# Performance work log

Hardware: AMD Instinct MI355X
Metric: run time of the kernel (lower is better)

Reference implementation:

```python
import jax, jax.numpy as jnp
import numpy as np

N_NODES = 50000
N_EDGES = 800000
IN_DIM, HIDDEN, Z_DIM = 32, 64, 32


def gcn_conv(x, W, b, src, dst, n):
    """PyG-style GCNConv: h = D^{-1/2}(A+I)D^{-1/2} (x W) + b."""
    h = x @ W  # [N, out]
    loop = jnp.arange(n, dtype=src.dtype)
    s = jnp.concatenate([src, loop])  # add self-loops
    d = jnp.concatenate([dst, loop])
    deg = jax.ops.segment_sum(jnp.ones(s.shape, h.dtype), d, num_segments=n)
    dinv = jax.lax.rsqrt(jnp.maximum(deg, jnp.asarray(1.0, h.dtype)))
    norm = dinv[s] * dinv[d]                       # [E+N]
    msg = h[s] * norm[:, None]                     # gather + scale
    out = jax.ops.segment_sum(msg, d, num_segments=n)  # scatter-add
    return out + b


def setup_inputs() -> dict:
    key = jax.random.key(0)
    ks = jax.random.split(key, 8)
    sc = lambda fan_in: 1.0 / np.sqrt(fan_in)
    x = jax.random.normal(ks[0], (N_NODES, IN_DIM), jnp.float32)
    edge_index = jax.random.randint(ks[1], (2, N_EDGES), 0, N_NODES, jnp.int64)
    W1 = jax.random.normal(ks[2], (IN_DIM, HIDDEN), jnp.float32) * sc(IN_DIM)
    b1 = jnp.zeros((HIDDEN,), jnp.float32)
    W2 = jax.random.normal(ks[3], (HIDDEN, HIDDEN), jnp.float32) * sc(HIDDEN)
    b2 = jnp.zeros((HIDDEN,), jnp.float32)
    W_mu = jax.random.normal(ks[4], (HIDDEN, Z_DIM), jnp.float32) * sc(HIDDEN)
    b_mu = jnp.zeros((Z_DIM,), jnp.float32)
    W_lv = jax.random.normal(ks[5], (HIDDEN, Z_DIM), jnp.float32) * sc(HIDDEN)
    b_lv = jnp.zeros((Z_DIM,), jnp.float32)
    eps = jax.random.normal(ks[6], (N_NODES, Z_DIM), jnp.float32)
    return {"x": x, "edge_index": edge_index, "W1": W1, "b1": b1, "W2": W2,
            "b2": b2, "W_mu": W_mu, "b_mu": b_mu, "W_lv": W_lv, "b_lv": b_lv,
            "eps": eps}


def reference(x, edge_index, W1, b1, W2, b2, W_mu, b_mu, W_lv, b_lv, eps):
    src, dst = edge_index[0], edge_index[1]
    n = x.shape[0]
    h = jax.nn.relu(gcn_conv(x, W1, b1, src, dst, n))
    h = jax.nn.relu(gcn_conv(h, W2, b2, src, dst, n))
    # dropout p=0.0 -> identity
    mu = gcn_conv(h, W_mu, b_mu, src, dst, n)
    logvar = gcn_conv(h, W_lv, b_lv, src, dst, n)
    z = mu + jnp.exp(0.5 * logvar) * eps  # reparametrize
    return (z, mu, logvar)
```

## Files before the change

### kernel.cpp

```cpp
#include <hip/hip_runtime.h>
#include <math.h>

#define N_NODES 50000
#define N_EDGES 800000
#define IN_DIM 32
#define HIDDEN 64
#define Z_DIM 32
#define SCAN_B 256
#define NB_SCAN ((N_NODES + SCAN_B - 1) / SCAN_B)
#define N_XCD 8
#define NPX ((N_NODES + N_XCD - 1) / N_XCD)
#define SLICE 2048
#define N_SLICE ((N_EDGES + SLICE - 1) / SLICE)
#define SCAT_B (N_SLICE * N_XCD)
#define FB 2048

__device__ __forceinline__ float bf2f(unsigned short u) {
    return __uint_as_float(((unsigned int)u) << 16);
}
__device__ __forceinline__ unsigned short f2bf(float f) {
    unsigned int u = __float_as_uint(f);
    u += 0x7fffu + ((u >> 16) & 1u);
    return (unsigned short)(u >> 16);
}

__device__ __forceinline__ int detect64(const int* raw) {
    int lane = threadIdx.x & 63;
    int odd = raw[2 * lane + 1];
    unsigned long long b = __ballot(odd != 0);
    return (b == 0ULL) ? 1 : 0;
}

__global__ void prep_kernel(const float* __restrict__ x, unsigned short* __restrict__ xb,
                            const void* __restrict__ raw, int* __restrict__ flag,
                            int* __restrict__ cnt, int2* __restrict__ ep0) {
    int is64 = detect64((const int*)raw);
    int i = blockIdx.x * 256 + threadIdx.x;
    if (blockIdx.x == 0 && threadIdx.x == 0) *flag = is64;
    if (i < N_NODES * IN_DIM) xb[i] = f2bf(x[i]);
    if (blockIdx.x < SCAT_B) {
        int xcd = blockIdx.x % N_XCD;
        int sl  = blockIdx.x / N_XCD;
        int own = ((sl % N_XCD) == xcd) ? 1 : 0;
        int lo  = xcd * NPX, hi = lo + NPX;
        int base = sl * SLICE;
#pragma unroll
        for (int j = 0; j < SLICE / 256; j++) {
            int e = base + j * 256 + threadIdx.x;
            if (e < N_EDGES) {
                int d = is64 ? (int)((const long long*)raw)[N_EDGES + e]
                             : ((const int*)raw)[N_EDGES + e];
                if (own) {
                    int s = is64 ? (int)((const long long*)raw)[e]
                                 : ((const int*)raw)[e];
                    ep0[e] = make_int2(s, d);
                }
                if (d >= lo && d < hi) atomicAdd(&cnt[d], 1);
            }
        }
    }
}

__global__ void scan1_kernel(const int* __restrict__ cnt, int* __restrict__ pre,
                             int* __restrict__ bsum, float* __restrict__ dinv) {
    __shared__ int s[SCAN_B];
    int t = threadIdx.x;
    int g = blockIdx.x * SCAN_B + t;
    int v = (g < N_NODES) ? cnt[g] : 0;
    if (g < N_NODES) dinv[g] = rsqrtf((float)(v + 1));
    s[t] = v;
    __syncthreads();
    for (int o = 1; o < SCAN_B; o <<= 1) {
        int add = (t >= o) ? s[t - o] : 0;
        __syncthreads();
        s[t] += add;
        __syncthreads();
    }
    if (g < N_NODES) pre[g] = s[t] - v;
    if (t == SCAN_B - 1) bsum[blockIdx.x] = s[t];
}

__global__ void scan23_kernel(int* __restrict__ rowptr, const int* __restrict__ bsum,
                              int* __restrict__ cursor) {
    __shared__ int s[256];
    int t = threadIdx.x;
    int v = (t < NB_SCAN) ? bsum[t] : 0;
    s[t] = v;
    __syncthreads();
    for (int o = 1; o < 256; o <<= 1) {
        int add = (t >= o) ? s[t - o] : 0;
        __syncthreads();
        s[t] += add;
        __syncthreads();
    }
    int excl = s[blockIdx.x] - bsum[blockIdx.x];
    int g = blockIdx.x * SCAN_B + t;
    if (g < N_NODES) {
        int r = rowptr[g] + excl;
        rowptr[g] = r;
        cursor[g] = r;
    }
    if (g == 0) rowptr[N_NODES] = N_EDGES;
}

__global__ __launch_bounds__(256) void scatter_kernel(
        const int2* __restrict__ ep0, const float* __restrict__ dinv,
        int* __restrict__ cursor, int2* __restrict__ ep) {
    int xcd = blockIdx.x % N_XCD;
    int sl  = blockIdx.x / N_XCD;
    int lo  = xcd * NPX, hi = lo + NPX;
    int base = sl * SLICE;
#pragma unroll
    for (int j = 0; j < SLICE / 256; j++) {
        int e = base + j * 256 + threadIdx.x;
        if (e >= N_EDGES) continue;
        int2 sd = ep0[e];
        if (sd.y >= lo && sd.y < hi) {
            float w = dinv[sd.x];
            int p = atomicAdd(&cursor[sd.y], 1);
            ep[p] = make_int2(sd.x, __float_as_int(w));
        }
    }
}

__device__ __forceinline__ float2 agg_node64(int e0, int e1, int2 pr0,
                                             const int2* __restrict__ ep,
                                             const unsigned int* __restrict__ gw,
                                             int lane, float2 acc) {
    int half = lane >> 5;
    int col  = lane & 31;
    int2 pr = pr0;
    for (int base = e0; base < e1; base += 64) {
        int cnt = e1 - base; cnt = cnt > 64 ? 64 : cnt;
        int j = 0;
        for (; j + 16 <= cnt; j += 16) {
            unsigned int fv[8]; float wv[8];
#pragma unroll
            for (int u = 0; u < 8; u++) {
                int j0 = j + 2 * u;
                int sa = __builtin_amdgcn_readlane(pr.x, j0);
                int sb = __builtin_amdgcn_readlane(pr.x, j0 + 1);
                int wa = __builtin_amdgcn_readlane(pr.y, j0);
                int wb = __builtin_amdgcn_readlane(pr.y, j0 + 1);
                int s  = half ? sb : sa;
                wv[u]  = __int_as_float(half ? wb : wa);
                fv[u]  = gw[(size_t)s * 32 + col];
            }
#pragma unroll
            for (int u = 0; u < 8; u++) {
                acc.x = fmaf(wv[u], __uint_as_float(fv[u] << 16),          acc.x);
                acc.y = fmaf(wv[u], __uint_as_float(fv[u] & 0xffff0000u),  acc.y);
            }
        }
        for (; j < cnt; j += 8) {
            unsigned int fv[4]; float wv[4];
#pragma unroll
            for (int u = 0; u < 4; u++) {
                int j0 = j + 2 * u, j1 = j0 + 1;
                int ia = j0 < 63 ? j0 : 63;
                int ib = j1 < 63 ? j1 : 63;
                int sa = __builtin_amdgcn_readlane(pr.x, ia);
                int sb = __builtin_amdgcn_readlane(pr.x, ib);
                float wa = (j0 < cnt) ? __int_as_float(__builtin_amdgcn_readlane(pr.y, ia)) : 0.0f;
                float wb = (j1 < cnt) ? __int_as_float(__builtin_amdgcn_readlane(pr.y, ib)) : 0.0f;
                int s  = half ? sb : sa;
                wv[u]  = half ? wb : wa;
                fv[u]  = gw[(size_t)s * 32 + col];
            }
#pragma unroll
            for (int u = 0; u < 4; u++) {
                acc.x = fmaf(wv[u], __uint_as_float(fv[u] << 16),          acc.x);
                acc.y = fmaf(wv[u], __uint_as_float(fv[u] & 0xffff0000u),  acc.y);
            }
        }
        int nb = base + 64;
        if (nb < e1) {
            int idx = nb + lane;
            pr = ep[idx < N_EDGES ? idx : (N_EDGES - 1)];
        }
    }
    return acc;
}

__device__ __forceinline__ float2 agg_node32(int e0, int e1, int2 pr0,
                                             const int2* __restrict__ ep,
                                             const unsigned int* __restrict__ xw,
                                             int lane, float2 acc) {
    int qc  = lane >> 4;
    int col = lane & 15;
    int2 pr = pr0;
    for (int base = e0; base < e1; base += 64) {
        int cnt = e1 - base; cnt = cnt > 64 ? 64 : cnt;
        int j = 0;
        for (; j + 16 <= cnt; j += 16) {
            unsigned int fv[4]; float wv[4];
#pragma unroll
            for (int u = 0; u < 4; u++) {
                int j0 = j + 4 * u;
                int s0 = __builtin_amdgcn_readlane(pr.x, j0);
                int s1 = __builtin_amdgcn_readlane(pr.x, j0 + 1);
                int s2 = __builtin_amdgcn_readlane(pr.x, j0 + 2);
                int s3 = __builtin_amdgcn_readlane(pr.x, j0 + 3);
                int w0 = __builtin_amdgcn_readlane(pr.y, j0);
                int w1 = __builtin_amdgcn_readlane(pr.y, j0 + 1);
                int w2 = __builtin_amdgcn_readlane(pr.y, j0 + 2);
                int w3 = __builtin_amdgcn_readlane(pr.y, j0 + 3);
                int s  = qc == 0 ? s0 : qc == 1 ? s1 : qc == 2 ? s2 : s3;
                int w  = qc == 0 ? w0 : qc == 1 ? w1 : qc == 2 ? w2 : w3;
                wv[u]  = __int_as_float(w);
                fv[u]  = xw[(size_t)s * 16 + col];
            }
#pragma unroll
            for (int u = 0; u < 4; u++) {
                acc.x = fmaf(wv[u], __uint_as_float(fv[u] << 16),          acc.x);
                acc.y = fmaf(wv[u], __uint_as_float(fv[u] & 0xffff0000u),  acc.y);
            }
        }
        for (; j < cnt; j += 8) {
            unsigned int fv[2]; float wv[2];
#pragma unroll
            for (int u = 0; u < 2; u++) {
                int j0 = j + 4 * u;
                int i0 = j0     < 63 ? j0     : 63;
                int i1 = j0 + 1 < 63 ? j0 + 1 : 63;
                int i2 = j0 + 2 < 63 ? j0 + 2 : 63;
                int i3 = j0 + 3 < 63 ? j0 + 3 : 63;
                int s0 = __builtin_amdgcn_readlane(pr.x, i0);
                int s1 = __builtin_amdgcn_readlane(pr.x, i1);
                int s2 = __builtin_amdgcn_readlane(pr.x, i2);
                int s3 = __builtin_amdgcn_readlane(pr.x, i3);
                float w0 = (j0     < cnt) ? __int_as_float(__builtin_amdgcn_readlane(pr.y, i0)) : 0.0f;
                float w1 = (j0 + 1 < cnt) ? __int_as_float(__builtin_amdgcn_readlane(pr.y, i1)) : 0.0f;
                float w2 = (j0 + 2 < cnt) ? __int_as_float(__builtin_amdgcn_readlane(pr.y, i2)) : 0.0f;
                float w3 = (j0 + 3 < cnt) ? __int_as_float(__builtin_amdgcn_readlane(pr.y, i3)) : 0.0f;
                int s  = qc == 0 ? s0 : qc == 1 ? s1 : qc == 2 ? s2 : s3;
                wv[u]  = qc == 0 ? w0 : qc == 1 ? w1 : qc == 2 ? w2 : w3;
                fv[u]  = xw[(size_t)s * 16 + col];
            }
#pragma unroll
            for (int u = 0; u < 2; u++) {
                acc.x = fmaf(wv[u], __uint_as_float(fv[u] << 16),          acc.x);
                acc.y = fmaf(wv[u], __uint_as_float(fv[u] & 0xffff0000u),  acc.y);
            }
        }
        int nb = base + 64;
        if (nb < e1) {
            int idx = nb + lane;
            pr = ep[idx < N_EDGES ? idx : (N_EDGES - 1)];
        }
    }
    return acc;
}

__global__ __launch_bounds__(256, 4) void fused_layer32_kernel(
        const int* __restrict__ rowptr, const int2* __restrict__ ep,
        const float* __restrict__ dinv, const unsigned short* __restrict__ xb,
        const float* __restrict__ W1, const float* __restrict__ b1,
        unsigned short* __restrict__ out) {
    __shared__ float sq[4 * 64];
    int lane = threadIdx.x & 63;
    int wav  = threadIdx.x >> 6;
    int qc   = lane >> 4;
    const unsigned int* xw = (const unsigned int*)xb;
    float wcol[IN_DIM];
#pragma unroll
    for (int k = 0; k < IN_DIM; k++) wcol[k] = W1[k * 64 + lane];
    float bb = b1[lane];
    int wid = __builtin_amdgcn_readfirstlane((int)((blockIdx.x * blockDim.x + threadIdx.x) >> 6));
    int nw  = (gridDim.x * blockDim.x) >> 6;
    int v = wid;
    if (v >= N_NODES) return;
    int e0 = rowptr[v], e1 = rowptr[v + 1];
    float dv = dinv[v];
    unsigned int hv = xw[(size_t)v * 16 + (lane & 15)];
    int i0 = e0 + lane;
    int2 pr = ep[i0 < N_EDGES ? i0 : (N_EDGES - 1)];
    while (v < N_NODES) {
        int vn = v + nw;
        int e0n = 0, e1n = 0;
        float dvn = 0.0f;
        unsigned int hvn = 0;
        int2 prn = make_int2(0, 0);
        if (vn < N_NODES) {
            e0n = rowptr[vn]; e1n = rowptr[vn + 1];
            dvn = dinv[vn];
            hvn = xw[(size_t)vn * 16 + (lane & 15)];
            int in0 = e0n + lane;
            prn = ep[in0 < N_EDGES ? in0 : (N_EDGES - 1)];
        }
        float sv = (qc == 0) ? dv : 0.0f;
        float2 acc;
        acc.x = sv * __uint_as_float(hv << 16);
        acc.y = sv * __uint_as_float(hv & 0xffff0000u);
        acc = agg_node32(e0, e1, pr, ep, xw, lane, acc);
        acc.x += __shfl_xor(acc.x, 16);
        acc.y += __shfl_xor(acc.y, 16);
        acc.x += __shfl_xor(acc.x, 32);
        acc.y += __shfl_xor(acc.y, 32);
        float qx = dv * acc.x, qy = dv * acc.y;
        if (lane < 16) ((float2*)sq)[wav * 32 + lane] = make_float2(qx, qy);
        float o = bb;
        const float4* q4 = (const float4*)(sq + wav * 64);
#pragma unroll
        for (int c = 0; c < IN_DIM / 4; c++) {
            float4 t = q4[c];
            o = fmaf(t.x, wcol[4 * c + 0], o);
            o = fmaf(t.y, wcol[4 * c + 1], o);
            o = fmaf(t.z, wcol[4 * c + 2], o);
            o = fmaf(t.w, wcol[4 * c + 3], o);
        }
        out[(size_t)v * 64 + lane] = f2bf(fmaxf(o, 0.0f));
        v = vn; e0 = e0n; e1 = e1n; dv = dvn; hv = hvn; pr = prn;
    }
}

__global__ __launch_bounds__(256, 4) void fused_layer64_kernel(
        const int* __restrict__ rowptr, const int2* __restrict__ ep,
        const float* __restrict__ dinv, const unsigned short* __restrict__ g,
        const float* __restrict__ W, const float* __restrict__ bias,
        unsigned short* __restrict__ out) {
    __shared__ float sq[4 * 64];
    int lane = threadIdx.x & 63;
    int wav  = threadIdx.x >> 6;
    int half = lane >> 5;
    const unsigned int* gw = (const unsigned int*)g;
    float wcol[HIDDEN];
#pragma unroll
    for (int k = 0; k < HIDDEN; k++) wcol[k] = W[k * 64 + lane];
    float bb = bias[lane];
    int wid = __builtin_amdgcn_readfirstlane((int)((blockIdx.x * blockDim.x + threadIdx.x) >> 6));
    int nw  = (gridDim.x * blockDim.x) >> 6;
    int v = wid;
    if (v >= N_NODES) return;
    int e0 = rowptr[v], e1 = rowptr[v + 1];
    float dv = dinv[v];
    unsigned int hv = gw[(size_t)v * 32 + (lane & 31)];
    int i0 = e0 + lane;
    int2 pr = ep[i0 < N_EDGES ? i0 : (N_EDGES - 1)];
    while (v < N_NODES) {
        int vn = v + nw;
        int e0n = 0, e1n = 0;
        float dvn = 0.0f;
        unsigned int hvn = 0;
        int2 prn = make_int2(0, 0);
        if (vn < N_NODES) {
            e0n = rowptr[vn]; e1n = rowptr[vn + 1];
            dvn = dinv[vn];
            hvn = gw[(size_t)vn * 32 + (lane & 31)];
            int in0 = e0n + lane;
            prn = ep[in0 < N_EDGES ? in0 : (N_EDGES - 1)];
        }
        float sv = half ? 0.0f : dv;
        float2 acc;
        acc.x = sv * __uint_as_float(hv << 16);
        acc.y = sv * __uint_as_float(hv & 0xffff0000u);
        acc = agg_node64(e0, e1, pr, ep, gw, lane, acc);
        acc.x += __shfl_xor(acc.x, 32);
        acc.y += __shfl_xor(acc.y, 32);
        float qx = dv * acc.x, qy = dv * acc.y;
        if (lane < 32) ((float2*)sq)[wav * 32 + lane] = make_float2(qx, qy);
        float o = bb;
        const float4* q4 = (const float4*)(sq + wav * 64);
#pragma unroll
        for (int c = 0; c < HIDDEN / 4; c++) {
            float4 t = q4[c];
            o = fmaf(t.x, wcol[4 * c + 0], o);
            o = fmaf(t.y, wcol[4 * c + 1], o);
            o = fmaf(t.z, wcol[4 * c + 2], o);
            o = fmaf(t.w, wcol[4 * c + 3], o);
        }
        out[(size_t)v * 64 + lane] = f2bf(fmaxf(o, 0.0f));
        v = vn; e0 = e0n; e1 = e1n; dv = dvn; hv = hvn; pr = prn;
    }
}

__global__ __launch_bounds__(256, 4) void fused_head_kernel(
        const int* __restrict__ rowptr, const int2* __restrict__ ep,
        const float* __restrict__ dinv, const unsigned short* __restrict__ g,
        const float* __restrict__ Wmu, const float* __restrict__ Wlv,
        const float* __restrict__ bmu, const float* __restrict__ blv,
        const float* __restrict__ eps, float* __restrict__ outz) {
    __shared__ float sq[4 * 64];
    int lane = threadIdx.x & 63;
    int wav  = threadIdx.x >> 6;
    int half = lane >> 5;
    int f = lane & 31;
    bool hi = lane >= 32;
    const unsigned int* gw = (const unsigned int*)g;
    float wcol[HIDDEN];
#pragma unroll
    for (int k = 0; k < HIDDEN; k++)
        wcol[k] = hi ? Wlv[k * 32 + f] : Wmu[k * 32 + f];
    float bb = hi ? blv[f] : bmu[f];
    float* z  = outz;
    float* mu = outz + (size_t)N_NODES * Z_DIM;
    float* lv = outz + 2 * (size_t)N_NODES * Z_DIM;
    int wid = __builtin_amdgcn_readfirstlane((int)((blockIdx.x * blockDim.x + threadIdx.x) >> 6));
    int nw  = (gridDim.x * blockDim.x) >> 6;
    int v = wid;
    if (v >= N_NODES) return;
    int e0 = rowptr[v], e1 = rowptr[v + 1];
    float dv = dinv[v];
    unsigned int hv = gw[(size_t)v * 32 + (lane & 31)];
    int i0 = e0 + lane;
    int2 pr = ep[i0 < N_EDGES ? i0 : (N_EDGES - 1)];
    while (v < N_NODES) {
        int vn = v + nw;
        int e0n = 0, e1n = 0;
        float dvn = 0.0f;
        unsigned int hvn = 0;
        int2 prn = make_int2(0, 0);
        if (vn < N_NODES) {
            e0n = rowptr[vn]; e1n = rowptr[vn + 1];
            dvn = dinv[vn];
            hvn = gw[(size_t)vn * 32 + (lane & 31)];
            int in0 = e0n + lane;
            prn = ep[in0 < N_EDGES ? in0 : (N_EDGES - 1)];
        }
        float sv = half ? 0.0f : dv;
        float2 acc;
        acc.x = sv * __uint_as_float(hv << 16);
        acc.y = sv * __uint_as_float(hv & 0xffff0000u);
        acc = agg_node64(e0, e1, pr, ep, gw, lane, acc);
        acc.x += __shfl_xor(acc.x, 32);
        acc.y += __shfl_xor(acc.y, 32);
        float qx = dv * acc.x, qy = dv * acc.y;
        if (lane < 32) ((float2*)sq)[wav * 32 + lane] = make_float2(qx, qy);
        float m = bb;
        const float4* q4 = (const float4*)(sq + wav * 64);
#pragma unroll
        for (int c = 0; c < HIDDEN / 4; c++) {
            float4 t = q4[c];
            m = fmaf(t.x, wcol[4 * c + 0], m);
            m = fmaf(t.y, wcol[4 * c + 1], m);
            m = fmaf(t.z, wcol[4 * c + 2], m);
            m = fmaf(t.w, wcol[4 * c + 3], m);
        }
        float ev = eps[(size_t)v * Z_DIM + f];
        float t  = expf(0.5f * m) * ev;
        float tlo = __shfl(t, lane | 32);
        size_t o = (size_t)v * Z_DIM + f;
        if (!hi) { mu[o] = m; z[o] = m + tlo; }
        else     { lv[o] = m; }
        v = vn; e0 = e0n; e1 = e1n; dv = dvn; hv = hvn; pr = prn;
    }
}

extern "C" void kernel_launch(void* const* d_in, const int* in_sizes, int n_in,
                              void* d_out, int out_size, void* d_ws, size_t ws_size,
                              hipStream_t stream) {
    const float* x   = (const float*)d_in[0];
    const void*  ei  = d_in[1];
    const float* W1  = (const float*)d_in[2];
    const float* b1  = (const float*)d_in[3];
    const float* W2  = (const float*)d_in[4];
    const float* b2  = (const float*)d_in[5];
    const float* Wmu = (const float*)d_in[6];
    const float* bmu = (const float*)d_in[7];
    const float* Wlv = (const float*)d_in[8];
    const float* blv = (const float*)d_in[9];
    const float* eps = (const float*)d_in[10];
    float* out = (float*)d_out;
    (void)in_sizes; (void)n_in; (void)out_size; (void)ws_size;

    char* ws = (char*)d_ws;
    size_t off = 0;
    auto alloc = [&](size_t bytes) -> void* {
        void* p = ws + off;
        off += (bytes + 255) & ~(size_t)255;
        return p;
    };
    int2*           ep     = (int2*)alloc(sizeof(int2) * N_EDGES);
    int2*           ep0    = (int2*)alloc(sizeof(int2) * N_EDGES);
    int*            rowptr = (int*)alloc(sizeof(int) * (N_NODES + 1));
    int*            cursor = (int*)alloc(sizeof(int) * N_NODES);
    int*            cnt    = (int*)alloc(sizeof(int) * N_NODES);
    float*          dinv   = (float*)alloc(sizeof(float) * N_NODES);
    int*            flag   = (int*)alloc(sizeof(int) * 64);
    int*            bsum   = (int*)alloc(sizeof(int) * 256);
    unsigned short* xb     = (unsigned short*)alloc(sizeof(short) * (size_t)N_NODES * IN_DIM);
    unsigned short* G      = (unsigned short*)alloc(sizeof(short) * (size_t)N_NODES * HIDDEN);
    unsigned short* H      = (unsigned short*)alloc(sizeof(short) * (size_t)N_NODES * HIDDEN);

    hipMemsetAsync(cnt, 0, sizeof(int) * N_NODES, stream);
    prep_kernel<<<(N_NODES * IN_DIM + 255) / 256, 256, 0, stream>>>(x, xb, ei, flag, cnt, ep0);
    scan1_kernel<<<NB_SCAN, SCAN_B, 0, stream>>>(cnt, rowptr, bsum, dinv);
    scan23_kernel<<<NB_SCAN, SCAN_B, 0, stream>>>(rowptr, bsum, cursor);
    scatter_kernel<<<SCAT_B, 256, 0, stream>>>(ep0, dinv, cursor, ep);
    fused_layer32_kernel<<<FB, 256, 0, stream>>>(rowptr, ep, dinv, xb, W1, b1, H);
    fused_layer64_kernel<<<FB, 256, 0, stream>>>(rowptr, ep, dinv, H, W2, b2, G);
    fused_head_kernel<<<FB, 256, 0, stream>>>(rowptr, ep, dinv, G, Wmu, Wlv, bmu, blv, eps, out);
}
```

Before: 274.2 us.

## Record atomic rank in count pass; widen gather lanes to 8-byte loads

The degree-count pass now stores each edge's atomic return value as its rank, so the CSR scatter becomes a plain rowptr+rank write with no second atomic pass and no per-XCD filtering. The aggregation loops now give each lane 4 bf16 features through 8-byte loads, with more edges in flight per wave. Edge indices are broadcast with ds_bpermute instead of chains of readlane, and the tail loop is merged into the main loop using clamped indices. This costs an extra rank array and more shuffle reductions per node, and the scatter now spans all destinations, so its writes may have worse locality.

```diff
diff --git a/kernel.cpp b/kernel.cpp
--- a/kernel.cpp
+++ b/kernel.cpp
@@ -33,7 +33,8 @@
 
 __global__ void prep_kernel(const float* __restrict__ x, unsigned short* __restrict__ xb,
                             const void* __restrict__ raw, int* __restrict__ flag,
-                            int* __restrict__ cnt, int2* __restrict__ ep0) {
+                            int* __restrict__ cnt, int2* __restrict__ ep0,
+                            int* __restrict__ rank) {
     int is64 = detect64((const int*)raw);
     int i = blockIdx.x * 256 + threadIdx.x;
     if (blockIdx.x == 0 && threadIdx.x == 0) *flag = is64;
@@ -55,7 +56,7 @@
                                  : ((const int*)raw)[e];
                     ep0[e] = make_int2(s, d);
                 }
-                if (d >= lo && d < hi) atomicAdd(&cnt[d], 1);
+                if (d >= lo && d < hi) rank[e] = atomicAdd(&cnt[d], 1);
             }
         }
     }
@@ -80,8 +81,7 @@
     if (t == SCAN_B - 1) bsum[blockIdx.x] = s[t];
 }
 
-__global__ void scan23_kernel(int* __restrict__ rowptr, const int* __restrict__ bsum,
-                              int* __restrict__ cursor) {
+__global__ void scan23_kernel(int* __restrict__ rowptr, const int* __restrict__ bsum) {
     __shared__ int s[256];
     int t = threadIdx.x;
     int v = (t < NB_SCAN) ? bsum[t] : 0;
@@ -95,82 +95,51 @@
     }
     int excl = s[blockIdx.x] - bsum[blockIdx.x];
     int g = blockIdx.x * SCAN_B + t;
-    if (g < N_NODES) {
-        int r = rowptr[g] + excl;
-        rowptr[g] = r;
-        cursor[g] = r;
-    }
+    if (g < N_NODES) rowptr[g] += excl;
     if (g == 0) rowptr[N_NODES] = N_EDGES;
 }
 
 __global__ __launch_bounds__(256) void scatter_kernel(
-        const int2* __restrict__ ep0, const float* __restrict__ dinv,
-        int* __restrict__ cursor, int2* __restrict__ ep) {
-    int xcd = blockIdx.x % N_XCD;
-    int sl  = blockIdx.x / N_XCD;
-    int lo  = xcd * NPX, hi = lo + NPX;
-    int base = sl * SLICE;
+        const int2* __restrict__ ep0, const int* __restrict__ rank,
+        const int* __restrict__ rowptr, const float* __restrict__ dinv,
+        int2* __restrict__ ep) {
+    int base = blockIdx.x * SLICE;
 #pragma unroll
     for (int j = 0; j < SLICE / 256; j++) {
         int e = base + j * 256 + threadIdx.x;
-        if (e >= N_EDGES) continue;
-        int2 sd = ep0[e];
-        if (sd.y >= lo && sd.y < hi) {
-            float w = dinv[sd.x];
-            int p = atomicAdd(&cursor[sd.y], 1);
-            ep[p] = make_int2(sd.x, __float_as_int(w));
-        }
-    }
-}
-
-__device__ __forceinline__ float2 agg_node64(int e0, int e1, int2 pr0,
-                                             const int2* __restrict__ ep,
-                                             const unsigned int* __restrict__ gw,
-                                             int lane, float2 acc) {
-    int half = lane >> 5;
-    int col  = lane & 31;
-    int2 pr = pr0;
+        if (e < N_EDGES) {
+            int2 sd = ep0[e];
+            int p = rowptr[sd.y] + rank[e];
+            ep[p] = make_int2(sd.x, __float_as_int(dinv[sd.x]));
+        }
+    }
+}
+
+__device__ __forceinline__ void agg_body64(int e0, int e1, int2 pr,
+                                           const int2* __restrict__ ep,
+                                           const uint2* __restrict__ g2,
+                                           int lane, float acc[4]) {
+    int gsel = lane >> 4;
+    int c    = lane & 15;
     for (int base = e0; base < e1; base += 64) {
         int cnt = e1 - base; cnt = cnt > 64 ? 64 : cnt;
-        int j = 0;
-        for (; j + 16 <= cnt; j += 16) {
-            unsigned int fv[8]; float wv[8];
-#pragma unroll
-            for (int u = 0; u < 8; u++) {
-                int j0 = j + 2 * u;
-                int sa = __builtin_amdgcn_readlane(pr.x, j0);
-                int sb = __builtin_amdgcn_readlane(pr.x, j0 + 1);
-                int wa = __builtin_amdgcn_readlane(pr.y, j0);
-                int wb = __builtin_amdgcn_readlane(pr.y, j0 + 1);
-                int s  = half ? sb : sa;
-                wv[u]  = __int_as_float(half ? wb : wa);
-                fv[u]  = gw[(size_t)s * 32 + col];
+        for (int j = 0; j < cnt; j += 16) {
+            uint2 fv[4]; float wv[4];
+#pragma unroll
+            for (int u = 0; u < 4; u++) {
+                int idx = j + u * 4 + gsel;
+                int cl  = idx < cnt ? idx : cnt - 1;
+                int s   = __builtin_amdgcn_ds_bpermute(cl << 2, pr.x);
+                int w   = __builtin_amdgcn_ds_bpermute(cl << 2, pr.y);
+                wv[u]   = idx < cnt ? __int_as_float(w) : 0.0f;
+                fv[u]   = g2[(size_t)s * 16 + c];
             }
 #pragma unroll
-            for (int u = 0; u < 8; u++) {
-                acc.x = fmaf(wv[u], __uint_as_float(fv[u] << 16),          acc.x);
-                acc.y = fmaf(wv[u], __uint_as_float(fv[u] & 0xffff0000u),  acc.y);
-            }
-        }
-        for (; j < cnt; j += 8) {
-            unsigned int fv[4]; float wv[4];
-#pragma unroll
             for (int u = 0; u < 4; u++) {
-                int j0 = j + 2 * u, j1 = j0 + 1;
-                int ia = j0 < 63 ? j0 : 63;
-                int ib = j1 < 63 ? j1 : 63;
-                int sa = __builtin_amdgcn_readlane(pr.x, ia);
-                int sb = __builtin_amdgcn_readlane(pr.x, ib);
-                float wa = (j0 < cnt) ? __int_as_float(__builtin_amdgcn_readlane(pr.y, ia)) : 0.0f;
-                float wb = (j1 < cnt) ? __int_as_float(__builtin_amdgcn_readlane(pr.y, ib)) : 0.0f;
-                int s  = half ? sb : sa;
-                wv[u]  = half ? wb : wa;
-                fv[u]  = gw[(size_t)s * 32 + col];
-            }
-#pragma unroll
-            for (int u = 0; u < 4; u++) {
-                acc.x = fmaf(wv[u], __uint_as_float(fv[u] << 16),          acc.x);
-                acc.y = fmaf(wv[u], __uint_as_float(fv[u] & 0xffff0000u),  acc.y);
+                acc[0] = fmaf(wv[u], __uint_as_float(fv[u].x << 16),         acc[0]);
+                acc[1] = fmaf(wv[u], __uint_as_float(fv[u].x & 0xffff0000u), acc[1]);
+                acc[2] = fmaf(wv[u], __uint_as_float(fv[u].y << 16),         acc[2]);
+                acc[3] = fmaf(wv[u], __uint_as_float(fv[u].y & 0xffff0000u), acc[3]);
             }
         }
         int nb = base + 64;
@@ -179,68 +148,33 @@
             pr = ep[idx < N_EDGES ? idx : (N_EDGES - 1)];
         }
     }
-    return acc;
-}
-
-__device__ __forceinline__ float2 agg_node32(int e0, int e1, int2 pr0,
-                                             const int2* __restrict__ ep,
-                                             const unsigned int* __restrict__ xw,
-                                             int lane, float2 acc) {
-    int qc  = lane >> 4;
-    int col = lane & 15;
-    int2 pr = pr0;
+}
+
+__device__ __forceinline__ void agg_body32(int e0, int e1, int2 pr,
+                                           const int2* __restrict__ ep,
+                                           const uint2* __restrict__ x2,
+                                           int lane, float acc[4]) {
+    int gsel = lane >> 3;
+    int c    = lane & 7;
     for (int base = e0; base < e1; base += 64) {
         int cnt = e1 - base; cnt = cnt > 64 ? 64 : cnt;
-        int j = 0;
-        for (; j + 16 <= cnt; j += 16) {
-            unsigned int fv[4]; float wv[4];
-#pragma unroll
-            for (int u = 0; u < 4; u++) {
-                int j0 = j + 4 * u;
-                int s0 = __builtin_amdgcn_readlane(pr.x, j0);
-                int s1 = __builtin_amdgcn_readlane(pr.x, j0 + 1);
-                int s2 = __builtin_amdgcn_readlane(pr.x, j0 + 2);
-                int s3 = __builtin_amdgcn_readlane(pr.x, j0 + 3);
-                int w0 = __builtin_amdgcn_readlane(pr.y, j0);
-                int w1 = __builtin_amdgcn_readlane(pr.y, j0 + 1);
-                int w2 = __builtin_amdgcn_readlane(pr.y, j0 + 2);
-                int w3 = __builtin_amdgcn_readlane(pr.y, j0 + 3);
-                int s  = qc == 0 ? s0 : qc == 1 ? s1 : qc == 2 ? s2 : s3;
-                int w  = qc == 0 ? w0 : qc == 1 ? w1 : qc == 2 ? w2 : w3;
-                wv[u]  = __int_as_float(w);
-                fv[u]  = xw[(size_t)s * 16 + col];
+        for (int j = 0; j < cnt; j += 16) {
+            uint2 fv[2]; float wv[2];
+#pragma unroll
+            for (int u = 0; u < 2; u++) {
+                int idx = j + u * 8 + gsel;
+                int cl  = idx < cnt ? idx : cnt - 1;
+                int s   = __builtin_amdgcn_ds_bpermute(cl << 2, pr.x);
+                int w   = __builtin_amdgcn_ds_bpermute(cl << 2, pr.y);
+                wv[u]   = idx < cnt ? __int_as_float(w) : 0.0f;
+                fv[u]   = x2[(size_t)s * 8 + c];
             }
 #pragma unroll
-            for (int u = 0; u < 4; u++) {
-                acc.x = fmaf(wv[u], __uint_as_float(fv[u] << 16),          acc.x);
-                acc.y = fmaf(wv[u], __uint_as_float(fv[u] & 0xffff0000u),  acc.y);
-            }
-        }
-        for (; j < cnt; j += 8) {
-            unsigned int fv[2]; float wv[2];
-#pragma unroll
             for (int u = 0; u < 2; u++) {
-                int j0 = j + 4 * u;
-                int i0 = j0     < 63 ? j0     : 63;
-                int i1 = j0 + 1 < 63 ? j0 + 1 : 63;
-                int i2 = j0 + 2 < 63 ? j0 + 2 : 63;
-                int i3 = j0 + 3 < 63 ? j0 + 3 : 63;
-                int s0 = __builtin_amdgcn_readlane(pr.x, i0);
-                int s1 = __builtin_amdgcn_readlane(pr.x, i1);
-                int s2 = __builtin_amdgcn_readlane(pr.x, i2);
-                int s3 = __builtin_amdgcn_readlane(pr.x, i3);
-                float w0 = (j0     < cnt) ? __int_as_float(__builtin_amdgcn_readlane(pr.y, i0)) : 0.0f;
-                float w1 = (j0 + 1 < cnt) ? __int_as_float(__builtin_amdgcn_readlane(pr.y, i1)) : 0.0f;
-                float w2 = (j0 + 2 < cnt) ? __int_as_float(__builtin_amdgcn_readlane(pr.y, i2)) : 0.0f;
-                float w3 = (j0 + 3 < cnt) ? __int_as_float(__builtin_amdgcn_readlane(pr.y, i3)) : 0.0f;
-                int s  = qc == 0 ? s0 : qc == 1 ? s1 : qc == 2 ? s2 : s3;
-                wv[u]  = qc == 0 ? w0 : qc == 1 ? w1 : qc == 2 ? w2 : w3;
-                fv[u]  = xw[(size_t)s * 16 + col];
-            }
-#pragma unroll
-            for (int u = 0; u < 2; u++) {
-                acc.x = fmaf(wv[u], __uint_as_float(fv[u] << 16),          acc.x);
-                acc.y = fmaf(wv[u], __uint_as_float(fv[u] & 0xffff0000u),  acc.y);
+                acc[0] = fmaf(wv[u], __uint_as_float(fv[u].x << 16),         acc[0]);
+                acc[1] = fmaf(wv[u], __uint_as_float(fv[u].x & 0xffff0000u), acc[1]);
+                acc[2] = fmaf(wv[u], __uint_as_float(fv[u].y << 16),         acc[2]);
+                acc[3] = fmaf(wv[u], __uint_as_float(fv[u].y & 0xffff0000u), acc[3]);
             }
         }
         int nb = base + 64;
@@ -249,7 +183,6 @@
             pr = ep[idx < N_EDGES ? idx : (N_EDGES - 1)];
         }
     }
-    return acc;
 }
 
 __global__ __launch_bounds__(256, 4) void fused_layer32_kernel(
@@ -257,11 +190,12 @@
         const float* __restrict__ dinv, const unsigned short* __restrict__ xb,
         const float* __restrict__ W1, const float* __restrict__ b1,
         unsigned short* __restrict__ out) {
-    __shared__ float sq[4 * 64];
+    __shared__ float sq[4 * 32];
     int lane = threadIdx.x & 63;
     int wav  = threadIdx.x >> 6;
-    int qc   = lane >> 4;
-    const unsigned int* xw = (const unsigned int*)xb;
+    int gsel = lane >> 3;
+    int c    = lane & 7;
+    const uint2* x2 = (const uint2*)xb;
     float wcol[IN_DIM];
 #pragma unroll
     for (int k = 0; k < IN_DIM; k++) wcol[k] = W1[k * 64 + lane];
@@ -272,42 +206,47 @@
     if (v >= N_NODES) return;
     int e0 = rowptr[v], e1 = rowptr[v + 1];
     float dv = dinv[v];
-    unsigned int hv = xw[(size_t)v * 16 + (lane & 15)];
+    uint2 hv = x2[(size_t)v * 8 + c];
     int i0 = e0 + lane;
     int2 pr = ep[i0 < N_EDGES ? i0 : (N_EDGES - 1)];
     while (v < N_NODES) {
         int vn = v + nw;
         int e0n = 0, e1n = 0;
         float dvn = 0.0f;
-        unsigned int hvn = 0;
+        uint2 hvn = make_uint2(0, 0);
         int2 prn = make_int2(0, 0);
         if (vn < N_NODES) {
             e0n = rowptr[vn]; e1n = rowptr[vn + 1];
             dvn = dinv[vn];
-            hvn = xw[(size_t)vn * 16 + (lane & 15)];
+            hvn = x2[(size_t)vn * 8 + c];
             int in0 = e0n + lane;
             prn = ep[in0 < N_EDGES ? in0 : (N_EDGES - 1)];
         }
-        float sv = (qc == 0) ? dv : 0.0f;
-        float2 acc;
-        acc.x = sv * __uint_as_float(hv << 16);
-        acc.y = sv * __uint_as_float(hv & 0xffff0000u);
-        acc = agg_node32(e0, e1, pr, ep, xw, lane, acc);
-        acc.x += __shfl_xor(acc.x, 16);
-        acc.y += __shfl_xor(acc.y, 16);
-        acc.x += __shfl_xor(acc.x, 32);
-        acc.y += __shfl_xor(acc.y, 32);
-        float qx = dv * acc.x, qy = dv * acc.y;
-        if (lane < 16) ((float2*)sq)[wav * 32 + lane] = make_float2(qx, qy);
+        float sv = (gsel == 0) ? dv : 0.0f;
+        float acc[4];
+        acc[0] = sv * __uint_as_float(hv.x << 16);
+        acc[1] = sv * __uint_as_float(hv.x & 0xffff0000u);
+        acc[2] = sv * __uint_as_float(hv.y << 16);
+        acc[3] = sv * __uint_as_float(hv.y & 0xffff0000u);
+        agg_body32(e0, e1, pr, ep, x2, lane, acc);
+#pragma unroll
+        for (int i = 0; i < 4; i++) {
+            acc[i] += __shfl_xor(acc[i], 8);
+            acc[i] += __shfl_xor(acc[i], 16);
+            acc[i] += __shfl_xor(acc[i], 32);
+        }
+        if (lane < 8)
+            ((float4*)(sq + wav * 32))[c] =
+                make_float4(dv * acc[0], dv * acc[1], dv * acc[2], dv * acc[3]);
         float o = bb;
-        const float4* q4 = (const float4*)(sq + wav * 64);
-#pragma unroll
-        for (int c = 0; c < IN_DIM / 4; c++) {
-            float4 t = q4[c];
-            o = fmaf(t.x, wcol[4 * c + 0], o);
-            o = fmaf(t.y, wcol[4 * c + 1], o);
-            o = fmaf(t.z, wcol[4 * c + 2], o);
-            o = fmaf(t.w, wcol[4 * c + 3], o);
+        const float4* q4 = (const float4*)(sq + wav * 32);
+#pragma unroll
+        for (int k = 0; k < IN_DIM / 4; k++) {
+            float4 t = q4[k];
+            o = fmaf(t.x, wcol[4 * k + 0], o);
+            o = fmaf(t.y, wcol[4 * k + 1], o);
+            o = fmaf(t.z, wcol[4 * k + 2], o);
+            o = fmaf(t.w, wcol[4 * k + 3], o);
         }
         out[(size_t)v * 64 + lane] = f2bf(fmaxf(o, 0.0f));
         v = vn; e0 = e0n; e1 = e1n; dv = dvn; hv = hvn; pr = prn;
@@ -322,8 +261,9 @@
     __shared__ float sq[4 * 64];
     int lane = threadIdx.x & 63;
     int wav  = threadIdx.x >> 6;
-    int half = lane >> 5;
-    const unsigned int* gw = (const unsigned int*)g;
+    int gsel = lane >> 4;
+    int c    = lane & 15;
+    const uint2* g2 = (const uint2*)g;
     float wcol[HIDDEN];
 #pragma unroll
     for (int k = 0; k < HIDDEN; k++) wcol[k] = W[k * 64 + lane];
@@ -334,40 +274,46 @@
     if (v >= N_NODES) return;
     int e0 = rowptr[v], e1 = rowptr[v + 1];
     float dv = dinv[v];
-    unsigned int hv = gw[(size_t)v * 32 + (lane & 31)];
+    uint2 hv = g2[(size_t)v * 16 + c];
     int i0 = e0 + lane;
     int2 pr = ep[i0 < N_EDGES ? i0 : (N_EDGES - 1)];
     while (v < N_NODES) {
         int vn = v + nw;
         int e0n = 0, e1n = 0;
         float dvn = 0.0f;
-        unsigned int hvn = 0;
+        uint2 hvn = make_uint2(0, 0);
         int2 prn = make_int2(0, 0);
         if (vn < N_NODES) {
             e0n = rowptr[vn]; e1n = rowptr[vn + 1];
             dvn = dinv[vn];
-            hvn = gw[(size_t)vn * 32 + (lane & 31)];
+            hvn = g2[(size_t)vn * 16 + c];
             int in0 = e0n + lane;
             prn = ep[in0 < N_EDGES ? in0 : (N_EDGES - 1)];
         }
-        float sv = half ? 0.0f : dv;
-        float2 acc;
-        acc.x = sv * __uint_as_float(hv << 16);
-        acc.y = sv * __uint_as_float(hv & 0xffff0000u);
-        acc = agg_node64(e0, e1, pr, ep, gw, lane, acc);
-        acc.x += __shfl_xor(acc.x, 32);
-        acc.y += __shfl_xor(acc.y, 32);
-        float qx = dv * acc.x, qy = dv * acc.y;
-        if (lane < 32) ((float2*)sq)[wav * 32 + lane] = make_float2(qx, qy);
+        float sv = (gsel == 0) ? dv : 0.0f;
+        float acc[4];
+        acc[0] = sv * __uint_as_float(hv.x << 16);
+        acc[1] = sv * __uint_as_float(hv.x & 0xffff0000u);
+        acc[2] = sv * __uint_as_float(hv.y << 16);
+        acc[3] = sv * __uint_as_float(hv.y & 0xffff0000u);
+        agg_body64(e0, e1, pr, ep, g2, lane, acc);
+#pragma unroll
+        for (int i = 0; i < 4; i++) {
+            acc[i] += __shfl_xor(acc[i], 16);
+            acc[i] += __shfl_xor(acc[i], 32);
+        }
+        if (lane < 16)
+            ((float4*)(sq + wav * 64))[c] =
+                make_float4(dv * acc[0], dv * acc[1], dv * acc[2], dv * acc[3]);
         float o = bb;
         const float4* q4 = (const float4*)(sq + wav * 64);
 #pragma unroll
-        for (int c = 0; c < HIDDEN / 4; c++) {
-            float4 t = q4[c];
-            o = fmaf(t.x, wcol[4 * c + 0], o);
-            o = fmaf(t.y, wcol[4 * c + 1], o);
-            o = fmaf(t.z, wcol[4 * c + 2], o);
-            o = fmaf(t.w, wcol[4 * c + 3], o);
+        for (int k = 0; k < HIDDEN / 4; k++) {
+            float4 t = q4[k];
+            o = fmaf(t.x, wcol[4 * k + 0], o);
+            o = fmaf(t.y, wcol[4 * k + 1], o);
+            o = fmaf(t.z, wcol[4 * k + 2], o);
+            o = fmaf(t.w, wcol[4 * k + 3], o);
         }
         out[(size_t)v * 64 + lane] = f2bf(fmaxf(o, 0.0f));
         v = vn; e0 = e0n; e1 = e1n; dv = dvn; hv = hvn; pr = prn;
@@ -383,10 +329,11 @@
     __shared__ float sq[4 * 64];
     int lane = threadIdx.x & 63;
     int wav  = threadIdx.x >> 6;
-    int half = lane >> 5;
+    int gsel = lane >> 4;
+    int c    = lane & 15;
     int f = lane & 31;
     bool hi = lane >= 32;
-    const unsigned int* gw = (const unsigned int*)g;
+    const uint2* g2 = (const uint2*)g;
     float wcol[HIDDEN];
 #pragma unroll
     for (int k = 0; k < HIDDEN; k++)
@@ -401,40 +348,46 @@
     if (v >= N_NODES) return;
     int e0 = rowptr[v], e1 = rowptr[v + 1];
     float dv = dinv[v];
-    unsigned int hv = gw[(size_t)v * 32 + (lane & 31)];
+    uint2 hv = g2[(size_t)v * 16 + c];
     int i0 = e0 + lane;
     int2 pr = ep[i0 < N_EDGES ? i0 : (N_EDGES - 1)];
     while (v < N_NODES) {
         int vn = v + nw;
         int e0n = 0, e1n = 0;
         float dvn = 0.0f;
-        unsigned int hvn = 0;
+        uint2 hvn = make_uint2(0, 0);
         int2 prn = make_int2(0, 0);
         if (vn < N_NODES) {
             e0n = rowptr[vn]; e1n = rowptr[vn + 1];
             dvn = dinv[vn];
-            hvn = gw[(size_t)vn * 32 + (lane & 31)];
+            hvn = g2[(size_t)vn * 16 + c];
             int in0 = e0n + lane;
             prn = ep[in0 < N_EDGES ? in0 : (N_EDGES - 1)];
         }
-        float sv = half ? 0.0f : dv;
-        float2 acc;
-        acc.x = sv * __uint_as_float(hv << 16);
-        acc.y = sv * __uint_as_float(hv & 0xffff0000u);
-        acc = agg_node64(e0, e1, pr, ep, gw, lane, acc);
-        acc.x += __shfl_xor(acc.x, 32);
-        acc.y += __shfl_xor(acc.y, 32);
-        float qx = dv * acc.x, qy = dv * acc.y;
-        if (lane < 32) ((float2*)sq)[wav * 32 + lane] = make_float2(qx, qy);
+        float sv = (gsel == 0) ? dv : 0.0f;
+        float acc[4];
+        acc[0] = sv * __uint_as_float(hv.x << 16);
+        acc[1] = sv * __uint_as_float(hv.x & 0xffff0000u);
+        acc[2] = sv * __uint_as_float(hv.y << 16);
+        acc[3] = sv * __uint_as_float(hv.y & 0xffff0000u);
+        agg_body64(e0, e1, pr, ep, g2, lane, acc);
+#pragma unroll
+        for (int i = 0; i < 4; i++) {
+            acc[i] += __shfl_xor(acc[i], 16);
+            acc[i] += __shfl_xor(acc[i], 32);
+        }
+        if (lane < 16)
+            ((float4*)(sq + wav * 64))[c] =
+                make_float4(dv * acc[0], dv * acc[1], dv * acc[2], dv * acc[3]);
         float m = bb;
         const float4* q4 = (const float4*)(sq + wav * 64);
 #pragma unroll
-        for (int c = 0; c < HIDDEN / 4; c++) {
-            float4 t = q4[c];
-            m = fmaf(t.x, wcol[4 * c + 0], m);
-            m = fmaf(t.y, wcol[4 * c + 1], m);
-            m = fmaf(t.z, wcol[4 * c + 2], m);
-            m = fmaf(t.w, wcol[4 * c + 3], m);
+        for (int k = 0; k < HIDDEN / 4; k++) {
+            float4 t = q4[k];
+            m = fmaf(t.x, wcol[4 * k + 0], m);
+            m = fmaf(t.y, wcol[4 * k + 1], m);
+            m = fmaf(t.z, wcol[4 * k + 2], m);
+            m = fmaf(t.w, wcol[4 * k + 3], m);
         }
         float ev = eps[(size_t)v * Z_DIM + f];
         float t  = expf(0.5f * m) * ev;
@@ -472,8 +425,8 @@
     };
     int2*           ep     = (int2*)alloc(sizeof(int2) * N_EDGES);
     int2*           ep0    = (int2*)alloc(sizeof(int2) * N_EDGES);
+    int*            rank   = (int*)alloc(sizeof(int) * N_EDGES);
     int*            rowptr = (int*)alloc(sizeof(int) * (N_NODES + 1));
-    int*            cursor = (int*)alloc(sizeof(int) * N_NODES);
     int*            cnt    = (int*)alloc(sizeof(int) * N_NODES);
     float*          dinv   = (float*)alloc(sizeof(float) * N_NODES);
     int*            flag   = (int*)alloc(sizeof(int) * 64);
@@ -483,10 +436,10 @@
     unsigned short* H      = (unsigned short*)alloc(sizeof(short) * (size_t)N_NODES * HIDDEN);
 
     hipMemsetAsync(cnt, 0, sizeof(int) * N_NODES, stream);
-    prep_kernel<<<(N_NODES * IN_DIM + 255) / 256, 256, 0, stream>>>(x, xb, ei, flag, cnt, ep0);
+    prep_kernel<<<(N_NODES * IN_DIM + 255) / 256, 256, 0, stream>>>(x, xb, ei, flag, cnt, ep0, rank);
     scan1_kernel<<<NB_SCAN, SCAN_B, 0, stream>>>(cnt, rowptr, bsum, dinv);
-    scan23_kernel<<<NB_SCAN, SCAN_B, 0, stream>>>(rowptr, bsum, cursor);
-    scatter_kernel<<<SCAT_B, 256, 0, stream>>>(ep0, dinv, cursor, ep);
+    scan23_kernel<<<NB_SCAN, SCAN_B, 0, stream>>>(rowptr, bsum);
+    scatter_kernel<<<N_SLICE, 256, 0, stream>>>(ep0, rank, rowptr, dinv, ep);
     fused_layer32_kernel<<<FB, 256, 0, stream>>>(rowptr, ep, dinv, xb, W1, b1, H);
     fused_layer64_kernel<<<FB, 256, 0, stream>>>(rowptr, ep, dinv, H, W2, b2, G);
     fused_head_kernel<<<FB, 256, 0, stream>>>(rowptr, ep, dinv, G, Wmu, Wlv, bmu, blv, eps, out);
```

Result: faster. 231.2 us (-15.7%).
